# Kernel optimization log

Hardware: AMD Instinct MI355X
Metric: run time of the kernel (lower is better)

Reference implementation:

```python
import jax, jax.numpy as jnp
import numpy as np

# Config (matches init_kwargs)
L, K, N = 2048, 64, 8
CB, AB, G2 = 64, 8, 9
CSB, ASB, G3 = 16, 16, 3
ROUT_ITER = 3
B = 32
LN = L // N  # 256


def squash(s):
    sq = jnp.sum(s * s, axis=-1, keepdims=True)
    return sq / (1.0 + sq) * (s / jnp.sqrt(sq + 1e-8))


def conv1d(x, w, b, pad):
    # x: [B, Cin, L], w: [Cout, Cin, k]
    y = jax.lax.conv_general_dilated(x, w, window_strides=(1,), padding=[(pad, pad)],
                                     dimension_numbers=("NCH", "OIH", "NCH"))
    return y + b[None, :, None]


def routing(V, n_iters):
    # V: [B, Ln, n, cSB, aSB]
    b_logits = jnp.zeros(V.shape[:-1], dtype=V.dtype)
    v = None
    for r in range(n_iters):
        c = jax.nn.softmax(b_logits, axis=-1)[..., None]  # [B,Ln,n,cSB,1]
        s = jnp.sum(c * V, axis=-3)                        # [B,Ln,cSB,aSB]
        v = squash(s)
        if r < n_iters - 1:
            a = jnp.sum(V * v[..., None, :, :], axis=-1)   # [B,Ln,n,cSB]
            b_logits = b_logits + jax.lax.stop_gradient(a)
    return v


def setup_inputs() -> dict:
    key = jax.random.key(0)
    ks = jax.random.split(key, 7)
    x = jax.random.normal(ks[0], (B, K, L), dtype=jnp.float32)
    w0 = jax.random.normal(ks[1], (CB, K, 1), dtype=jnp.float32) * 0.05
    b0 = jnp.zeros((CB,), dtype=jnp.float32)
    w1 = jax.random.normal(ks[2], (CB * AB, CB, G2), dtype=jnp.float32) * 0.05
    b1 = jnp.zeros((CB * AB,), dtype=jnp.float32)
    w2 = jax.random.normal(ks[3], (CSB * ASB, 1, G3, CB * AB), dtype=jnp.float32) * 0.05
    b2 = jnp.zeros((CSB * ASB,), dtype=jnp.float32)
    return {"x": x, "w0": w0, "b0": b0, "w1": w1, "b1": b1, "w2": w2, "b2": b2}


def reference(x, w0, b0, w1, b1, w2, b2):
    # convLayer: 1x1 conv1d  [B,K,L] -> [B,CB,L]
    h = conv1d(x, w0, b0, pad=0)
    # conv1: 'same' padding, odd kernel G2 -> symmetric pad G2//2
    h = conv1d(h, w1, b1, pad=G2 // 2)  # [B, CB*AB, L]
    # -> [B, Ln, n, CB*AB], squash primary capsules
    h = jnp.transpose(h, (0, 2, 1)).reshape(B, LN, N, CB * AB)
    h = squash(h)
    # -> [B, 1, Ln, n*CB*AB]
    h = h.reshape(B, LN, N * CB * AB)[:, None, :, :]
    # conv2: kernel (G3, CB*AB), stride (1, CB*AB), pad (G3//2, 0)
    pad_h = int(G3 / 2 - 0.5)
    h = jax.lax.conv_general_dilated(h, w2, window_strides=(1, CB * AB),
                                     padding=[(pad_h, pad_h), (0, 0)],
                                     dimension_numbers=("NCHW", "OIHW", "NCHW"))
    h = h + b2[None, :, None, None]                  # [B, CSB*ASB, Ln, n]
    V = jnp.transpose(h, (0, 2, 3, 1)).reshape(B, LN, N, CSB, ASB)
    v = routing(V, ROUT_ITER)                        # [B, Ln, CSB, ASB]
    return v.reshape(B, LN * CSB, ASB)
```

## Files before the change

kernel.cpp:

```cpp
#include <hip/hip_runtime.h>


#define LL    2048
#define NCAP  8
#define CO1   512
#define CO2   256
#define LNN   256

typedef __attribute__((ext_vector_type(8))) short bhalf8;
typedef __attribute__((ext_vector_type(4))) float facc4;

#define MFMA16(a, b, c) __builtin_amdgcn_mfma_f32_16x16x32_bf16(a, b, c, 0, 0, 0)

__device__ inline unsigned short f2bf(float f) {
  unsigned u = __float_as_uint(f);
  return (unsigned short)((u + 0x7FFFu + ((u >> 16) & 1u)) >> 16);
}

#if __has_builtin(__builtin_amdgcn_global_load_lds)
#define HAVE_GLDS 1
#else
#define HAVE_GLDS 0
#endif

__device__ __forceinline__ void g2l_lane(const unsigned short* g_lane,
                                         unsigned short* l_base, int lane) {
#if HAVE_GLDS
  __builtin_amdgcn_global_load_lds(
      (const __attribute__((address_space(1))) void*)g_lane,
      (__attribute__((address_space(3))) void*)l_base, 16, 0, 0);
#else
  *(bhalf8*)(l_base + lane * 8) = *(const bhalf8*)g_lane;
#endif
}

#define OFF_W1TB 0u
#define OFF_W2P  589824u
#define OFF_H0T  1474560u
#define OFF_H1   9863168u
#define OFF_H1SQ 144080896u

__global__ __launch_bounds__(256) void prep_kernel(
    const float* __restrict__ w1, const float* __restrict__ w2,
    unsigned short* __restrict__ w1tb, unsigned short* __restrict__ w2p) {
  int idx = blockIdx.x * 256 + threadIdx.x;
  if (idx < 294912) {
    int cb = idx & 63;
    int co = (idx >> 6) & 511;
    int g  = idx >> 15;
    w1tb[idx] = f2bf(w1[(co * 64 + cb) * 9 + g]);
  } else {
    int j = idx - 294912;
    int ci = j & 63;
    int t  = j >> 6;
    int o  = t & 255;
    t >>= 8;
    int g  = t % 3;
    int cc = t / 3;
    w2p[((cc * 3 + g) * 256 + o) * 64 + ci] =
        f2bf(w2[(o * 3 + g) * 512 + cc * 64 + ci]);
  }
}

__global__ __launch_bounds__(256) void conv0_kernel(
    const float* __restrict__ x, const float* __restrict__ w0,
    const float* __restrict__ b0, unsigned short* __restrict__ h0t) {
  __shared__ __align__(16) float xt[64][128];
  __shared__ __align__(16) float w0t[64][68];
  int tid = threadIdx.x;
  int b = blockIdx.y;
  int l0 = blockIdx.x * 128;
  const float* xb = x + (size_t)b * 64 * LL;
#pragma unroll
  for (int i = 0; i < 8; i++) {
    int idx = i * 256 + tid;
    int k = idx >> 5, l4 = idx & 31;
    float4 v = *(const float4*)&xb[k * LL + l0 + l4 * 4];
    *(float4*)&xt[k][l4 * 4] = v;
  }
#pragma unroll
  for (int i = 0; i < 16; i++) {
    int idx = i * 256 + tid;
    int cb = idx >> 6, k = idx & 63;
    w0t[k][cb] = w0[idx];
  }
  __syncthreads();
  int lc = tid & 31, rc = tid >> 5;
  float acc[8][4] = {};
  for (int k = 0; k < 64; k++) {
    float4 bv = *(const float4*)&xt[k][lc * 4];
    float4 a0 = *(const float4*)&w0t[k][rc * 8];
    float4 a1 = *(const float4*)&w0t[k][rc * 8 + 4];
    float a[8] = {a0.x, a0.y, a0.z, a0.w, a1.x, a1.y, a1.z, a1.w};
    float bb4[4] = {bv.x, bv.y, bv.z, bv.w};
#pragma unroll
    for (int i = 0; i < 8; i++)
#pragma unroll
      for (int j = 0; j < 4; j++) acc[i][j] += a[i] * bb4[j];
  }
  float bias[8];
#pragma unroll
  for (int i = 0; i < 8; i++) bias[i] = b0[rc * 8 + i];
#pragma unroll
  for (int j = 0; j < 4; j++) {
    bhalf8 o;
#pragma unroll
    for (int i = 0; i < 8; i++) o[i] = (short)f2bf(acc[i][j] + bias[i]);
    *(bhalf8*)&h0t[((size_t)b * LL + l0 + lc * 4 + j) * 64 + rc * 8] = o;
  }
}

__global__ __launch_bounds__(512) void conv1_mfma(
    const unsigned short* __restrict__ h0t, const unsigned short* __restrict__ w1tb,
    const float* __restrict__ b1, float* __restrict__ h1) {
  __shared__ __align__(16) unsigned short Xt[136 * 72];
  __shared__ __align__(16) unsigned short Wg[256 * 72];
  int tid = threadIdx.x;
  int b = blockIdx.z;
  int co0 = blockIdx.y * 256;
  int l0 = blockIdx.x * 128;
#pragma unroll
  for (int it = 0; it < 3; it++) {
    int idx = it * 512 + tid;
    if (idx < 1088) {
      int row = idx >> 3, c8 = (idx & 7) * 8;
      int l = l0 - 4 + row;
      bhalf8 v = (bhalf8)0;
      if (l >= 0 && l < LL) v = *(const bhalf8*)&h0t[((size_t)b * LL + l) * 64 + c8];
      *(bhalf8*)&Xt[row * 72 + c8] = v;
    }
  }
  int wid = tid >> 6, lane = tid & 63;
  int wr = wid >> 1, wc = wid & 1;
  int r16 = lane & 15, k8 = lane >> 4;
  facc4 acc[4][4] = {};
  for (int g = 0; g < 9; g++) {
    __syncthreads();
#pragma unroll
    for (int it = 0; it < 4; it++) {
      int idx = it * 512 + tid;
      int row = idx >> 3, c8 = (idx & 7) * 8;
      *(bhalf8*)&Wg[row * 72 + c8] =
          *(const bhalf8*)&w1tb[((size_t)(g * 512 + co0 + row)) * 64 + c8];
    }
    __syncthreads();
#pragma unroll
    for (int ks = 0; ks < 2; ks++) {
      bhalf8 A[4], Bf[4];
#pragma unroll
      for (int mi = 0; mi < 4; mi++)
        A[mi] = *(const bhalf8*)&Wg[(wr * 64 + mi * 16 + r16) * 72 + ks * 32 + k8 * 8];
#pragma unroll
      for (int ni = 0; ni < 4; ni++)
        Bf[ni] = *(const bhalf8*)&Xt[(wc * 64 + ni * 16 + r16 + g) * 72 + ks * 32 + k8 * 8];
#pragma unroll
      for (int mi = 0; mi < 4; mi++)
#pragma unroll
        for (int ni = 0; ni < 4; ni++)
          acc[mi][ni] = MFMA16(A[mi], Bf[ni], acc[mi][ni]);
    }
  }
#pragma unroll
  for (int mi = 0; mi < 4; mi++) {
    int co_w = co0 + wr * 64 + mi * 16 + k8 * 4;
    float4 bias = *(const float4*)&b1[co_w];
#pragma unroll
    for (int ni = 0; ni < 4; ni++) {
      int l_w = l0 + wc * 64 + ni * 16 + r16;
      float* p = &h1[((size_t)b * LL + l_w) * CO1 + co_w];
      *(float4*)p = make_float4(acc[mi][ni][0] + bias.x, acc[mi][ni][1] + bias.y,
                                acc[mi][ni][2] + bias.z, acc[mi][ni][3] + bias.w);
    }
  }
}

__global__ __launch_bounds__(256) void squash1_kernel(
    const float* __restrict__ h1, unsigned short* __restrict__ h1sq) {
  int tid = threadIdx.x;
  int wave = tid >> 6, lane = tid & 63;
  size_t row = (size_t)blockIdx.x * 4 + wave;
  const float* p = h1 + row * CO1;
  float4 v0 = *(const float4*)(p + lane * 8);
  float4 v1 = *(const float4*)(p + lane * 8 + 4);
  float sq = v0.x * v0.x + v0.y * v0.y + v0.z * v0.z + v0.w * v0.w +
             v1.x * v1.x + v1.y * v1.y + v1.z * v1.z + v1.w * v1.w;
#pragma unroll
  for (int m = 1; m < 64; m <<= 1) sq += __shfl_xor(sq, m, 64);
  float s = sq / (1.f + sq) / sqrtf(sq + 1e-8f);
  bhalf8 o;
  o[0] = (short)f2bf(v0.x * s); o[1] = (short)f2bf(v0.y * s);
  o[2] = (short)f2bf(v0.z * s); o[3] = (short)f2bf(v0.w * s);
  o[4] = (short)f2bf(v1.x * s); o[5] = (short)f2bf(v1.y * s);
  o[6] = (short)f2bf(v1.z * s); o[7] = (short)f2bf(v1.w * s);
  int b = (int)(row >> 11), l = (int)(row & 2047);
  int ln = l >> 3, n = l & 7;
  *(bhalf8*)&h1sq[((size_t)((b * 8 + n) * 256 + ln)) * 512 + lane * 8] = o;
}

__global__ __launch_bounds__(512) void conv2_mfma(
    const unsigned short* __restrict__ h1sq, const unsigned short* __restrict__ w2p,
    const float* __restrict__ b2, float* __restrict__ V) {
  __shared__ __align__(16) unsigned short HcA[258 * 64];
  __shared__ __align__(16) unsigned short HcB[258 * 64];
  __shared__ __align__(16) unsigned short WA[256 * 64];
  __shared__ __align__(16) unsigned short WB[256 * 64];
  int tid = threadIdx.x;
  int bn = blockIdx.x;
  int b = bn >> 3, n = bn & 7;
  int wid = tid >> 6, lane = tid & 63;
  int wr = wid >> 2, wc = wid & 3;
  int r16 = lane & 15, k8 = lane >> 4;
  int row8 = lane >> 3, slot = lane & 7;
  const unsigned short* hbase = h1sq + (size_t)(b * 8 + n) * 256 * 512;

  if (tid < 256) {
    int q = tid >> 6, c = tid & 63;
    unsigned short* hb = (q & 2) ? HcB : HcA;
    hb[((q & 1) ? 257 : 0) * 64 + c] = 0;
  }
  for (int ch = wid; ch < 32; ch += 8)
    g2l_lane(&w2p[(size_t)(ch * 8 + row8) * 64 + (slot ^ row8) * 8],
             &WA[ch * 8 * 64], lane);
  for (int ch = wid; ch < 32; ch += 8) {
    int r = 1 + ch * 8 + row8;
    g2l_lane(&hbase[(size_t)(r - 1) * 512 + (slot ^ (r & 7)) * 8],
             &HcA[(1 + ch * 8) * 64], lane);
  }
  __syncthreads();

  facc4 acc[8][4] = {};
  for (int p = 0; p < 24; ++p) {
    int g = p % 3, cc = p / 3;
    if (p < 23) {
      int pn = p + 1;
      int gn = pn % 3, ccn = pn / 3;
      unsigned short* Wd = (pn & 1) ? WB : WA;
      const unsigned short* wsrc = w2p + (size_t)(ccn * 3 + gn) * 16384;
      for (int ch = wid; ch < 32; ch += 8)
        g2l_lane(&wsrc[(size_t)(ch * 8 + row8) * 64 + (slot ^ row8) * 8],
                 &Wd[ch * 8 * 64], lane);
      if (gn == 0) {
        unsigned short* Hd = (ccn & 1) ? HcB : HcA;
        for (int ch = wid; ch < 32; ch += 8) {
          int r = 1 + ch * 8 + row8;
          g2l_lane(&hbase[(size_t)(r - 1) * 512 + ccn * 64 + (slot ^ (r & 7)) * 8],
                   &Hd[(1 + ch * 8) * 64], lane);
        }
      }
    }
    const unsigned short* Wc  = (p & 1) ? WB : WA;
    const unsigned short* Hcc = (cc & 1) ? HcB : HcA;
#pragma unroll
    for (int ks = 0; ks < 2; ++ks) {
      bhalf8 Av[8], Bv[4];
#pragma unroll
      for (int mi = 0; mi < 8; mi++) {
        int rw = wr * 128 + mi * 16 + r16;
        Av[mi] = *(const bhalf8*)&Wc[rw * 64 + ((ks * 4 + k8) ^ (r16 & 7)) * 8];
      }
#pragma unroll
      for (int ni = 0; ni < 4; ni++) {
        int rr = wc * 64 + ni * 16 + r16 + g;
        Bv[ni] = *(const bhalf8*)&Hcc[rr * 64 + ((ks * 4 + k8) ^ (rr & 7)) * 8];
      }
#pragma unroll
      for (int mi = 0; mi < 8; mi++)
#pragma unroll
        for (int ni = 0; ni < 4; ni++)
          acc[mi][ni] = MFMA16(Av[mi], Bv[ni], acc[mi][ni]);
    }
    __syncthreads();
  }
#pragma unroll
  for (int mi = 0; mi < 8; mi++) {
    int o_w = wr * 128 + mi * 16 + k8 * 4;
    float4 bias = *(const float4*)&b2[o_w];
#pragma unroll
    for (int ni = 0; ni < 4; ni++) {
      int ln_w = wc * 64 + ni * 16 + r16;
      float* p = &V[(((size_t)b * LNN + ln_w) * NCAP + n) * CO2 + o_w];
      *(float4*)p = make_float4(acc[mi][ni][0] + bias.x, acc[mi][ni][1] + bias.y,
                                acc[mi][ni][2] + bias.z, acc[mi][ni][3] + bias.w);
    }
  }
}

__global__ __launch_bounds__(256) void routing_kernel(
    const float* __restrict__ V, float* __restrict__ out) {
  __shared__ float Vs[8][16][17];
  __shared__ float blog[8][16];
  __shared__ float cbuf[8][16];
  __shared__ float vbuf[16][17];
  int tid = threadIdx.x;
  size_t base = (size_t)blockIdx.x * 2048;
#pragma unroll
  for (int i = 0; i < 8; i++) {
    int idx = i * 256 + tid;
    int nn = idx >> 8, r = idx & 255;
    Vs[nn][r >> 4][r & 15] = V[base + idx];
  }
  if (tid < 128) blog[tid >> 4][tid & 15] = 0.f;
  __syncthreads();
  int csb = tid >> 4, asb = tid & 15;
  for (int r = 0; r < 3; r++) {
    if (tid < 128) {
      int nn = tid >> 4, cs = tid & 15;
      float xv = blog[nn][cs];
      float m = xv;
#pragma unroll
      for (int d = 1; d < 16; d <<= 1) m = fmaxf(m, __shfl_xor(m, d, 16));
      float e = expf(xv - m);
      float ssum = e;
#pragma unroll
      for (int d = 1; d < 16; d <<= 1) ssum += __shfl_xor(ssum, d, 16);
      cbuf[nn][cs] = e / ssum;
    }
    __syncthreads();
    float s = 0.f;
#pragma unroll
    for (int q = 0; q < 8; q++) s += cbuf[q][csb] * Vs[q][csb][asb];
    float sq = s * s;
#pragma unroll
    for (int d = 1; d < 16; d <<= 1) sq += __shfl_xor(sq, d, 16);
    float vv = s * (sq / (1.f + sq) / sqrtf(sq + 1e-8f));
    if (r < 2) {
      vbuf[csb][asb] = vv;
      __syncthreads();
      if (tid < 128) {
        int nn = tid >> 4, cs = tid & 15;
        float a = 0.f;
#pragma unroll
        for (int q = 0; q < 16; q++) a += Vs[nn][cs][q] * vbuf[cs][q];
        blog[nn][cs] += a;
      }
      __syncthreads();
    } else {
      out[(size_t)blockIdx.x * 256 + tid] = vv;
    }
  }
}

extern "C" void kernel_launch(void* const* d_in, const int* in_sizes, int n_in,
                              void* d_out, int out_size, void* d_ws, size_t ws_size,
                              hipStream_t stream) {
  const float* x  = (const float*)d_in[0];
  const float* w0 = (const float*)d_in[1];
  const float* b0 = (const float*)d_in[2];
  const float* w1 = (const float*)d_in[3];
  const float* b1 = (const float*)d_in[4];
  const float* w2 = (const float*)d_in[5];
  const float* b2 = (const float*)d_in[6];
  float* out = (float*)d_out;
  char* ws = (char*)d_ws;
  unsigned short* w1tb = (unsigned short*)(ws + OFF_W1TB);
  unsigned short* w2p  = (unsigned short*)(ws + OFF_W2P);
  unsigned short* h0t  = (unsigned short*)(ws + OFF_H0T);
  float*          h1   = (float*)(ws + OFF_H1);
  unsigned short* h1sq = (unsigned short*)(ws + OFF_H1SQ);
  float*          Vb   = (float*)(ws + OFF_H1);

  prep_kernel<<<2688, 256, 0, stream>>>(w1, w2, w1tb, w2p);
  conv0_kernel<<<dim3(16, 32), 256, 0, stream>>>(x, w0, b0, h0t);
  conv1_mfma<<<dim3(16, 2, 32), 512, 0, stream>>>(h0t, w1tb, b1, h1);
  squash1_kernel<<<16384, 256, 0, stream>>>(h1, h1sq);
  conv2_mfma<<<256, 512, 0, stream>>>(h1sq, w2p, b2, Vb);
  routing_kernel<<<8192, 256, 0, stream>>>(Vb, out);
}
```

Before: 244.2 us.

## Fuse capsule squash into conv1 MFMA kernel with full-channel tiles

Conv1 now computes all 512 output channels per block, so the squash norm over channels can be reduced in-kernel through LDS. The squashed bf16 result is written directly to the conv2 layout, which removes the fp32 h1 round trip and the separate squash launch. Weight tiles are double-buffered with async global-to-LDS loads and XOR-swizzled LDS in place of padding. The cost is larger LDS use (about 150KB) and 128 accumulator registers per thread, which lowers occupancy, and the grid shrinks to 512 blocks.

```diff
diff --git a/kernel.cpp b/kernel.cpp
--- a/kernel.cpp
+++ b/kernel.cpp
@@ -110,91 +110,111 @@
   }
 }
 
-__global__ __launch_bounds__(512) void conv1_mfma(
+__global__ __launch_bounds__(512) void conv1_fused(
     const unsigned short* __restrict__ h0t, const unsigned short* __restrict__ w1tb,
-    const float* __restrict__ b1, float* __restrict__ h1) {
-  __shared__ __align__(16) unsigned short Xt[136 * 72];
-  __shared__ __align__(16) unsigned short Wg[256 * 72];
+    const float* __restrict__ b1, unsigned short* __restrict__ h1sq) {
+  __shared__ __align__(16) unsigned short Xt[136 * 64];
+  __shared__ __align__(16) unsigned short WA[512 * 64];
+  __shared__ __align__(16) unsigned short WB[512 * 64];
+  __shared__ float red[128][4];
+  __shared__ float scl[128];
   int tid = threadIdx.x;
-  int b = blockIdx.z;
-  int co0 = blockIdx.y * 256;
+  int b = blockIdx.y;
   int l0 = blockIdx.x * 128;
-#pragma unroll
-  for (int it = 0; it < 3; it++) {
-    int idx = it * 512 + tid;
-    if (idx < 1088) {
-      int row = idx >> 3, c8 = (idx & 7) * 8;
-      int l = l0 - 4 + row;
-      bhalf8 v = (bhalf8)0;
-      if (l >= 0 && l < LL) v = *(const bhalf8*)&h0t[((size_t)b * LL + l) * 64 + c8];
-      *(bhalf8*)&Xt[row * 72 + c8] = v;
-    }
-  }
   int wid = tid >> 6, lane = tid & 63;
   int wr = wid >> 1, wc = wid & 1;
   int r16 = lane & 15, k8 = lane >> 4;
-  facc4 acc[4][4] = {};
-  for (int g = 0; g < 9; g++) {
+  int row8 = lane >> 3, slot = lane & 7;
+  {
+    int hr = tid >> 6, c = tid & 63;
+    int row = (hr < 4) ? hr : 128 + hr;
+    int l = l0 - 4 + row;
+    unsigned short v = 0;
+    if (l >= 0 && l < LL) v = h0t[((size_t)b * LL + l) * 64 + c];
+    Xt[row * 64 + ((c >> 3) ^ (row & 7)) * 8 + (c & 7)] = v;
+  }
+  for (int ch = wid; ch < 16; ch += 8) {
+    int row = 4 + ch * 8 + row8;
+    g2l_lane(&h0t[((size_t)b * LL + (l0 - 4 + row)) * 64 + (slot ^ (row & 7)) * 8],
+             &Xt[(4 + ch * 8) * 64], lane);
+  }
+  for (int ch = wid; ch < 64; ch += 8)
+    g2l_lane(&w1tb[(size_t)(ch * 8 + row8) * 64 + (slot ^ row8) * 8],
+             &WA[ch * 8 * 64], lane);
+  __syncthreads();
+
+  facc4 acc[8][4] = {};
+  for (int g = 0; g < 9; ++g) {
+    if (g < 8) {
+      unsigned short* Wd = (g & 1) ? WA : WB;
+      const unsigned short* wsrc = w1tb + (size_t)(g + 1) * 512 * 64;
+      for (int ch = wid; ch < 64; ch += 8)
+        g2l_lane(&wsrc[(size_t)(ch * 8 + row8) * 64 + (slot ^ row8) * 8],
+                 &Wd[ch * 8 * 64], lane);
+    }
+    const unsigned short* Wc = (g & 1) ? WB : WA;
+#pragma unroll
+    for (int ks = 0; ks < 2; ++ks) {
+      bhalf8 Av[8], Bv[4];
+#pragma unroll
+      for (int mi = 0; mi < 8; mi++) {
+        int rw = wr * 128 + mi * 16 + r16;
+        Av[mi] = *(const bhalf8*)&Wc[rw * 64 + ((ks * 4 + k8) ^ (r16 & 7)) * 8];
+      }
+#pragma unroll
+      for (int ni = 0; ni < 4; ni++) {
+        int rr = wc * 64 + ni * 16 + r16 + g;
+        Bv[ni] = *(const bhalf8*)&Xt[rr * 64 + ((ks * 4 + k8) ^ (rr & 7)) * 8];
+      }
+#pragma unroll
+      for (int mi = 0; mi < 8; mi++)
+#pragma unroll
+        for (int ni = 0; ni < 4; ni++)
+          acc[mi][ni] = MFMA16(Av[mi], Bv[ni], acc[mi][ni]);
+    }
     __syncthreads();
-#pragma unroll
-    for (int it = 0; it < 4; it++) {
-      int idx = it * 512 + tid;
-      int row = idx >> 3, c8 = (idx & 7) * 8;
-      *(bhalf8*)&Wg[row * 72 + c8] =
-          *(const bhalf8*)&w1tb[((size_t)(g * 512 + co0 + row)) * 64 + c8];
-    }
-    __syncthreads();
-#pragma unroll
-    for (int ks = 0; ks < 2; ks++) {
-      bhalf8 A[4], Bf[4];
-#pragma unroll
-      for (int mi = 0; mi < 4; mi++)
-        A[mi] = *(const bhalf8*)&Wg[(wr * 64 + mi * 16 + r16) * 72 + ks * 32 + k8 * 8];
-#pragma unroll
-      for (int ni = 0; ni < 4; ni++)
-        Bf[ni] = *(const bhalf8*)&Xt[(wc * 64 + ni * 16 + r16 + g) * 72 + ks * 32 + k8 * 8];
-#pragma unroll
-      for (int mi = 0; mi < 4; mi++)
-#pragma unroll
-        for (int ni = 0; ni < 4; ni++)
-          acc[mi][ni] = MFMA16(A[mi], Bf[ni], acc[mi][ni]);
-    }
-  }
-#pragma unroll
-  for (int mi = 0; mi < 4; mi++) {
-    int co_w = co0 + wr * 64 + mi * 16 + k8 * 4;
+  }
+  float part[4] = {0.f, 0.f, 0.f, 0.f};
+#pragma unroll
+  for (int mi = 0; mi < 8; mi++) {
+    int co_w = wr * 128 + mi * 16 + k8 * 4;
     float4 bias = *(const float4*)&b1[co_w];
 #pragma unroll
     for (int ni = 0; ni < 4; ni++) {
-      int l_w = l0 + wc * 64 + ni * 16 + r16;
-      float* p = &h1[((size_t)b * LL + l_w) * CO1 + co_w];
-      *(float4*)p = make_float4(acc[mi][ni][0] + bias.x, acc[mi][ni][1] + bias.y,
-                                acc[mi][ni][2] + bias.z, acc[mi][ni][3] + bias.w);
-    }
-  }
-}
-
-__global__ __launch_bounds__(256) void squash1_kernel(
-    const float* __restrict__ h1, unsigned short* __restrict__ h1sq) {
-  int tid = threadIdx.x;
-  int wave = tid >> 6, lane = tid & 63;
-  size_t row = (size_t)blockIdx.x * 4 + wave;
-  const float* p = h1 + row * CO1;
-  float4 v0 = *(const float4*)(p + lane * 8);
-  float4 v1 = *(const float4*)(p + lane * 8 + 4);
-  float sq = v0.x * v0.x + v0.y * v0.y + v0.z * v0.z + v0.w * v0.w +
-             v1.x * v1.x + v1.y * v1.y + v1.z * v1.z + v1.w * v1.w;
-#pragma unroll
-  for (int m = 1; m < 64; m <<= 1) sq += __shfl_xor(sq, m, 64);
-  float s = sq / (1.f + sq) / sqrtf(sq + 1e-8f);
-  bhalf8 o;
-  o[0] = (short)f2bf(v0.x * s); o[1] = (short)f2bf(v0.y * s);
-  o[2] = (short)f2bf(v0.z * s); o[3] = (short)f2bf(v0.w * s);
-  o[4] = (short)f2bf(v1.x * s); o[5] = (short)f2bf(v1.y * s);
-  o[6] = (short)f2bf(v1.z * s); o[7] = (short)f2bf(v1.w * s);
-  int b = (int)(row >> 11), l = (int)(row & 2047);
-  int ln = l >> 3, n = l & 7;
-  *(bhalf8*)&h1sq[((size_t)((b * 8 + n) * 256 + ln)) * 512 + lane * 8] = o;
+      acc[mi][ni][0] += bias.x; acc[mi][ni][1] += bias.y;
+      acc[mi][ni][2] += bias.z; acc[mi][ni][3] += bias.w;
+      part[ni] += acc[mi][ni][0] * acc[mi][ni][0] + acc[mi][ni][1] * acc[mi][ni][1] +
+                  acc[mi][ni][2] * acc[mi][ni][2] + acc[mi][ni][3] * acc[mi][ni][3];
+    }
+  }
+#pragma unroll
+  for (int ni = 0; ni < 4; ni++) {
+    part[ni] += __shfl_xor(part[ni], 16, 64);
+    part[ni] += __shfl_xor(part[ni], 32, 64);
+    if (k8 == 0) red[wc * 64 + ni * 16 + r16][wr] = part[ni];
+  }
+  __syncthreads();
+  if (tid < 128) {
+    float sq = red[tid][0] + red[tid][1] + red[tid][2] + red[tid][3];
+    scl[tid] = sq / (1.f + sq) / sqrtf(sq + 1e-8f);
+  }
+  __syncthreads();
+#pragma unroll
+  for (int ni = 0; ni < 4; ni++) {
+    int l_loc = wc * 64 + ni * 16 + r16;
+    float s = scl[l_loc];
+    int l_w = l0 + l_loc;
+    int n = l_w & 7, ln = l_w >> 3;
+    size_t rbase = ((size_t)((b * 8 + n) * 256 + ln)) * 512;
+#pragma unroll
+    for (int mi = 0; mi < 8; mi++) {
+      int co_w = wr * 128 + mi * 16 + k8 * 4;
+      ushort4 o;
+      o.x = f2bf(acc[mi][ni][0] * s); o.y = f2bf(acc[mi][ni][1] * s);
+      o.z = f2bf(acc[mi][ni][2] * s); o.w = f2bf(acc[mi][ni][3] * s);
+      *(ushort4*)&h1sq[rbase + co_w] = o;
+    }
+  }
 }
 
 __global__ __launch_bounds__(512) void conv2_mfma(
@@ -355,14 +375,12 @@
   unsigned short* w1tb = (unsigned short*)(ws + OFF_W1TB);
   unsigned short* w2p  = (unsigned short*)(ws + OFF_W2P);
   unsigned short* h0t  = (unsigned short*)(ws + OFF_H0T);
-  float*          h1   = (float*)(ws + OFF_H1);
   unsigned short* h1sq = (unsigned short*)(ws + OFF_H1SQ);
   float*          Vb   = (float*)(ws + OFF_H1);
 
   prep_kernel<<<2688, 256, 0, stream>>>(w1, w2, w1tb, w2p);
   conv0_kernel<<<dim3(16, 32), 256, 0, stream>>>(x, w0, b0, h0t);
-  conv1_mfma<<<dim3(16, 2, 32), 512, 0, stream>>>(h0t, w1tb, b1, h1);
-  squash1_kernel<<<16384, 256, 0, stream>>>(h1, h1sq);
+  conv1_fused<<<dim3(16, 32), 512, 0, stream>>>(h0t, w1tb, b1, h1sq);
   conv2_mfma<<<256, 512, 0, stream>>>(h1sq, w2p, b2, Vb);
   routing_kernel<<<8192, 256, 0, stream>>>(Vb, out);
 }
```

Result: faster. 214.8 us (-12.0%).
